# Kernel tuning notes

Measured on AMD Instinct MI355X. Metric: run time of the kernel, lower is better.

## Reference

```python
import jax, jax.numpy as jnp
import numpy as np

S, T, C, L_GNN, L_TF, H = 8, 16, 128, 3, 2, 4
B = 512
FF = 4 * C
EPS = 1e-5


def setup_inputs() -> dict:
    key = jax.random.key(0)
    ks = jax.random.split(key, 24)
    w = lambda k, shape: jax.random.normal(k, shape, jnp.float32) * 0.05
    inp = {}
    inp["xx"] = jax.random.randint(ks[0], (B, T, S, S, S), 0, 3, dtype=jnp.int32)
    inp["ss"] = jax.random.uniform(ks[1], (B, 1), jnp.float32)
    # DynamicGNNv2 params
    inp["Win"] = w(ks[2], (C, 5)); inp["b_in"] = w(ks[3], (C,))
    inp["Wl"] = w(ks[4], (L_GNN, C, C)); inp["bl"] = w(ks[5], (L_GNN, C))   # SAGEConv lin_l (neighbors)
    inp["Wr"] = w(ks[6], (L_GNN, C, C))                                      # SAGEConv lin_r (root, no bias)
    inp["ln_g"] = jnp.ones((C,), jnp.float32); inp["ln_b"] = jnp.zeros((C,), jnp.float32)  # shared LayerNorm
    # TransformerEncoder params (norm_first, relu, dropout=0 at eval)
    inp["Wqkv"] = w(ks[7], (L_TF, 3 * C, C)); inp["bqkv"] = w(ks[8], (L_TF, 3 * C))
    inp["Wo"] = w(ks[9], (L_TF, C, C)); inp["bo"] = w(ks[10], (L_TF, C))
    inp["ln1_g"] = jnp.ones((L_TF, C), jnp.float32); inp["ln1_b"] = jnp.zeros((L_TF, C), jnp.float32)
    inp["ln2_g"] = jnp.ones((L_TF, C), jnp.float32); inp["ln2_b"] = jnp.zeros((L_TF, C), jnp.float32)
    inp["W1"] = w(ks[11], (L_TF, FF, C)); inp["b1"] = w(ks[12], (L_TF, FF))
    inp["W2"] = w(ks[13], (L_TF, C, FF)); inp["b2"] = w(ks[14], (L_TF, C))
    inp["Wact"] = w(ks[15], (C, S ** 3)); inp["bact"] = w(ks[16], (C,))
    inp["Wsc"] = w(ks[17], (C, 1)); inp["bsc"] = w(ks[18], (C,))
    return inp


def layernorm(x, g, b):
    mu = x.mean(-1, keepdims=True)
    var = ((x - mu) ** 2).mean(-1, keepdims=True)
    return (x - mu) * jax.lax.rsqrt(var + EPS) * g + b


def reference(xx, ss, Win, b_in, Wl, bl, Wr, ln_g, ln_b, Wqkv, bqkv, Wo, bo,
              ln1_g, ln1_b, ln2_g, ln2_b, W1, b1, W2, b2, Wact, bact, Wsc, bsc):
    Bc = xx.shape[0]
    S3 = S ** 3
    frame0 = xx[:, 0].reshape(Bc, S3).astype(jnp.float32)            # (B,S^3)
    m = (frame0 != 0).astype(jnp.float32)                            # active-node mask
    grid = jnp.arange(S3)
    i, j, k = grid // (S * S), (grid // S) % S, grid % S
    coord = jnp.stack([i, j, k], -1).astype(jnp.float32) / (S - 1)   # (S^3,3)
    feat = jnp.concatenate([
        jnp.broadcast_to(coord, (Bc, S3, 3)),
        (frame0 / 2.0)[..., None],
        jnp.broadcast_to((ss / S)[:, None, :], (Bc, S3, 1)),
    ], -1)                                                            # (B,S^3,5)
    x = feat @ Win.T + b_in                                           # lin_in
    mm = m[..., None]
    n = m.sum(-1, keepdims=True)[..., None]                           # nodes per graph (B,1,1)
    for l in range(L_GNN):
        # complete graph (no self loops): mean over neighbors = (sum_active - self)/(N-1)
        s = (x * mm).sum(1, keepdims=True)                            # (B,1,C)
        neigh = jnp.where(n > 1, (s - x) / jnp.maximum(n - 1.0, 1.0), 0.0)
        h = neigh @ Wl[l].T + bl[l] + x @ Wr[l].T                     # SAGEConv
        x = layernorm(jax.nn.relu(h), ln_g, ln_b)
    full = x * mm                                                     # scatter-fill into dense (B,S^3,C)
    # pooling matmul: mean over each i/j/k slice -> (B,3S,C)
    poolW = jnp.concatenate([
        (i[None, :] == jnp.arange(S)[:, None]).astype(jnp.float32),
        (j[None, :] == jnp.arange(S)[:, None]).astype(jnp.float32),
        (k[None, :] == jnp.arange(S)[:, None]).astype(jnp.float32),
    ], 0)                                                             # (3S,S^3)
    gnn_emb = jnp.einsum('ps,bsc->bpc', poolW, full) / poolW.sum(1)[None, :, None]
    # transformer over past actions
    a = xx[:, 1:].reshape(Bc, T - 1, S3).astype(jnp.float32) @ Wact.T + bact
    Hd = C // H
    scale = 1.0 / np.sqrt(Hd).astype(np.float32)
    split_heads = lambda t: t.reshape(Bc, -1, H, Hd).transpose(0, 2, 1, 3)
    for l in range(L_TF):
        h1 = layernorm(a, ln1_g[l], ln1_b[l])
        q, kk, v = jnp.split(h1 @ Wqkv[l].T + bqkv[l], 3, axis=-1)
        q, kk, v = split_heads(q), split_heads(kk), split_heads(v)
        att = jax.nn.softmax(jnp.einsum('bhqd,bhkd->bhqk', q, kk) * scale, -1)
        o = jnp.einsum('bhqk,bhkd->bhqd', att, v).transpose(0, 2, 1, 3).reshape(Bc, -1, C)
        a = a + (o @ Wo[l].T + bo[l])
        h2 = layernorm(a, ln2_g[l], ln2_b[l])
        a = a + (jax.nn.relu(h2 @ W1[l].T + b1[l]) @ W2[l].T + b2[l])
    act_emb = a.mean(1)                                               # (B,C)
    mv_emb = jax.nn.relu(ss @ Wsc.T + bsc)                            # (B,C)
    return jnp.concatenate([gnn_emb, act_emb[:, None], mv_emb[:, None]], 1)  # (B,3S+2,C)
```

## Files before the change

kernel.cpp:

```cpp
#include <hip/hip_runtime.h>
#include <hip/hip_bf16.h>
#include <string.h>

typedef __hip_bfloat16 bf16;
typedef __attribute__((ext_vector_type(8))) short short8;
typedef __attribute__((ext_vector_type(4))) float f32x4;

#define Bsz 512
#define S3  512
#define Tsz 16
#define Cc  128
#define TT  15
#define EPSv 1e-5f

__device__ __forceinline__ float u2f(unsigned short u) {
    return __uint_as_float(((unsigned)u) << 16);
}
__device__ __forceinline__ float ulo(unsigned u) { return __uint_as_float(u << 16); }
__device__ __forceinline__ float uhi(unsigned u) { return __uint_as_float(u & 0xffff0000u); }
__device__ __forceinline__ unsigned short f2bu(float v) {
    bf16 h = __float2bfloat16(v);
    unsigned short u; memcpy(&u, &h, 2); return u;
}
__device__ __forceinline__ unsigned short bfr16(float a) {
    unsigned u = __float_as_uint(a);
    u = u + 0x7fffu + ((u >> 16) & 1u);
    return (unsigned short)(u >> 16);
}
__device__ __forceinline__ unsigned fpack2(float a, float b) {
    unsigned ua = __float_as_uint(a), ub = __float_as_uint(b);
    ua = ua + 0x7fffu + ((ua >> 16) & 1u);
    ub = ub + 0x7fffu + ((ub >> 16) & 1u);
    return (ua >> 16) | (ub & 0xffff0000u);
}
__device__ __forceinline__ float dot4(float4 a, float4 b) {
    return a.x*b.x + a.y*b.y + a.z*b.z + a.w*b.w;
}

__global__ __launch_bounds__(256) void k_tpack(const float* __restrict__ src,
                                               float* __restrict__ dst,
                                               int NR, int NK)
{
    __shared__ float tile[32][33];
    int k0 = blockIdx.x * 32, r0 = blockIdx.y * 32;
    int lr = threadIdx.x >> 5, lk = threadIdx.x & 31;
    for (int i = lr; i < 32; i += 8)
        tile[i][lk] = src[(size_t)(r0 + i) * NK + k0 + lk];
    __syncthreads();
    int c = threadIdx.x & 31, k4 = threadIdx.x >> 5;
    float4 v;
    v.x = tile[c][k4 * 4 + 0]; v.y = tile[c][k4 * 4 + 1];
    v.z = tile[c][k4 * 4 + 2]; v.w = tile[c][k4 * 4 + 3];
    ((float4*)dst)[(size_t)(k0 / 4 + k4) * NR + r0 + c] = v;
}

__global__ __launch_bounds__(256) void k_cvt5(
    const float* __restrict__ s0, const float* __restrict__ s1,
    const float* __restrict__ s2, const float* __restrict__ s3,
    const float* __restrict__ s4, ushort* __restrict__ dst)
{
    int i = blockIdx.x * 256 + threadIdx.x;
    if (i >= 114688) return;
    const float* src; int rel;
    if (i < 16384)      { src = s0; rel = i; }
    else if (i < 40960) { src = s1; rel = i - 16384; }
    else if (i < 49152) { src = s2; rel = i - 40960; }
    else if (i < 81920) { src = s3; rel = i - 49152; }
    else                { src = s4; rel = i - 81920; }
    float4 v = ((const float4*)src)[rel];
    ushort4 o;
    o.x = f2bu(v.x); o.y = f2bu(v.y); o.z = f2bu(v.z); o.w = f2bu(v.w);
    ((ushort4*)dst)[i] = o;
}

__global__ __launch_bounds__(256) void k_dwall(
    const int* __restrict__ xx, const float* __restrict__ Wl,
    const float* __restrict__ Wr, ushort* __restrict__ dbuf)
{
    __shared__ float pc[4];
    __shared__ float winv;
    int b = blockIdx.x, l = blockIdx.y, tid = threadIdx.x;
    const int* x0 = xx + (size_t)b * Tsz * S3;
    int c = (x0[tid] != 0) + (x0[tid + 256] != 0);
    for (int off = 32; off; off >>= 1) c += __shfl_xor(c, off, 64);
    if ((tid & 63) == 0) pc[tid >> 6] = (float)c;
    __syncthreads();
    if (tid == 0) {
        float n = pc[0] + pc[1] + pc[2] + pc[3];
        winv = (n > 1.f) ? 1.f / (n - 1.f) : 0.f;
    }
    __syncthreads();
    float inv = winv;
    const float* wl = Wl + l * 16384;
    const float* wr = Wr + l * 16384;
    ushort* dst = dbuf + (size_t)(b * 3 + l) * 32 * 512;
    for (int item = tid; item < 2048; item += 256) {
        int f = item >> 6, lane = item & 63;
        int t = f >> 2, ks = f & 3, ml = lane & 15, q = lane >> 4;
        int n = t * 16 + ml, kb = ks * 32 + q * 8;
        const float4* wlr = (const float4*)(wl + n * 128 + kb);
        const float4* wrr = (const float4*)(wr + n * 128 + kb);
        float4 a0 = wlr[0], a1 = wlr[1];
        float4 r0 = wrr[0], r1 = wrr[1];
        ushort4 o0, o1;
        o0.x = f2bu(r0.x - inv * a0.x); o0.y = f2bu(r0.y - inv * a0.y);
        o0.z = f2bu(r0.z - inv * a0.z); o0.w = f2bu(r0.w - inv * a0.w);
        o1.x = f2bu(r1.x - inv * a1.x); o1.y = f2bu(r1.y - inv * a1.y);
        o1.z = f2bu(r1.z - inv * a1.z); o1.w = f2bu(r1.w - inv * a1.w);
        ushort* dp = dst + (size_t)f * 512 + lane * 8;
        *(ushort4*)dp = o0;
        *(ushort4*)(dp + 4) = o1;
    }
}

__global__ __launch_bounds__(1024) void k_torso(
    const int* __restrict__ xx, const float* __restrict__ ss,
    const float* __restrict__ Win, const float* __restrict__ b_in,
    const ushort* __restrict__ dbuf,
    const float4* __restrict__ WlP, const float* __restrict__ blv,
    const float* __restrict__ lng, const float* __restrict__ lnb,
    float* __restrict__ out)
{
    __shared__ ushort X[512 * 136];
    __shared__ float  mC[512];
    __shared__ float  sred[16 * 128];
    __shared__ float  ssc[128];
    __shared__ float  sbase[128];
    __shared__ float  gln[128], bln[128];
    __shared__ float  scnt[16];
    __shared__ float  invS;

    int b = blockIdx.x, tid = threadIdx.x;
    int wv = tid >> 6, lane = tid & 63;
    int ml = lane & 15, quad = lane >> 4;

    {
        int g = wv, cp = lane;
        int co0 = 2 * cp, co1 = 2 * cp + 1;
        const int* x0 = xx + (size_t)b * Tsz * S3;
        float f4c = ss[b] * (1.0f / 8.0f);
        float a0 = Win[co0*5+0], a1 = Win[co0*5+1], a2 = Win[co0*5+2], a3 = Win[co0*5+3];
        float c0 = Win[co1*5+0], c1 = Win[co1*5+1], c2 = Win[co1*5+2], c3 = Win[co1*5+3];
        float ba = b_in[co0] + f4c * Win[co0*5+4];
        float bc = b_in[co1] + f4c * Win[co1*5+4];
        float sp0 = 0.f, sp1 = 0.f; int cnt = 0;
        for (int node = g; node < S3; node += 16) {
            int f0 = x0[node];
            float m = (f0 != 0) ? 1.f : 0.f;
            float ci = (float)(node >> 6) * (1.f / 7.f);
            float cj = (float)((node >> 3) & 7) * (1.f / 7.f);
            float ck = (float)(node & 7) * (1.f / 7.f);
            float ft = (float)f0 * 0.5f;
            float v0 = ba + ci * a0 + cj * a1 + ck * a2 + ft * a3;
            float v1 = bc + ci * c0 + cj * c1 + ck * c2 + ft * c3;
            ((unsigned*)(X + node * 136))[cp] = fpack2(v0, v1);
            sp0 += v0 * m; sp1 += v1 * m;
            cnt += (f0 != 0);
            if (cp == 0) mC[node] = m;
        }
        sred[g * 128 + co0] = sp0;
        sred[g * 128 + co1] = sp1;
        if (cp == 0) scnt[g] = (float)cnt;
    }
    if (tid < 128) { gln[tid] = lng[tid]; bln[tid] = lnb[tid]; }
    __syncthreads();
    if (tid == 0) {
        float n = 0.f;
#pragma unroll
        for (int g = 0; g < 16; g++) n += scnt[g];
        invS = (n > 1.f) ? 1.f / (n - 1.f) : 0.f;
    }
    __syncthreads();
    if (tid < 128) {
        float s = 0.f;
#pragma unroll
        for (int g = 0; g < 16; g++) s += sred[g * 128 + tid];
        ssc[tid] = s * invS;
    }
    __syncthreads();
    if (tid < 128) {
        float a = blv[tid];
        for (int k4 = 0; k4 < 32; k4++)
            a += dot4(*(const float4*)(ssc + k4 * 4), WlP[k4 * 384 + tid]);
        sbase[tid] = a;
    }
    __syncthreads();

    for (int l = 0; l < 3; l++) {
        f32x4 acc[8][2];
#pragma unroll
        for (int t = 0; t < 8; t++)
#pragma unroll
            for (int m = 0; m < 2; m++) acc[t][m] = (f32x4){0.f, 0.f, 0.f, 0.f};

        const ushort* dL  = dbuf + (size_t)(b * 3 + l) * 32 * 512 + lane * 8;
        const ushort* xr0 = X + (wv * 32 + ml) * 136 + quad * 8;
        const ushort* xr1 = xr0 + 16 * 136;

#pragma unroll
        for (int ks = 0; ks < 4; ks++) {
            short8 a0 = *(const short8*)(xr0 + ks * 32);
            short8 a1 = *(const short8*)(xr1 + ks * 32);
            short8 bg0[4], bg1[4];
#pragma unroll
            for (int t = 0; t < 4; t++)
                bg0[t] = *(const short8*)(dL + (size_t)(t * 4 + ks) * 512);
#pragma unroll
            for (int t = 0; t < 4; t++)
                bg1[t] = *(const short8*)(dL + (size_t)((t + 4) * 4 + ks) * 512);
#pragma unroll
            for (int t = 0; t < 4; t++) {
                acc[t][0] = __builtin_amdgcn_mfma_f32_16x16x32_bf16(a0, bg0[t], acc[t][0], 0, 0, 0);
                acc[t][1] = __builtin_amdgcn_mfma_f32_16x16x32_bf16(a1, bg0[t], acc[t][1], 0, 0, 0);
            }
#pragma unroll
            for (int t = 0; t < 4; t++) {
                acc[t + 4][0] = __builtin_amdgcn_mfma_f32_16x16x32_bf16(a0, bg1[t], acc[t + 4][0], 0, 0, 0);
                acc[t + 4][1] = __builtin_amdgcn_mfma_f32_16x16x32_bf16(a1, bg1[t], acc[t + 4][1], 0, 0, 0);
            }
        }

        float bse[8], gg[8], be[8];
#pragma unroll
        for (int t = 0; t < 8; t++) {
            bse[t] = sbase[t * 16 + ml];
            gg[t]  = gln[t * 16 + ml];
            be[t]  = bln[t * 16 + ml];
        }
        float sp[8];
#pragma unroll
        for (int t = 0; t < 8; t++) sp[t] = 0.f;
        bool last = (l == 2);

#pragma unroll
        for (int m = 0; m < 2; m++) {
#pragma unroll
            for (int r = 0; r < 4; r++) {
                int row = wv * 32 + m * 16 + quad * 4 + r;
                float s = 0.f, q = 0.f;
#pragma unroll
                for (int t = 0; t < 8; t++) {
                    float v = fmaxf(acc[t][m][r] + bse[t], 0.f);
                    acc[t][m][r] = v;
                    s += v; q += v * v;
                }
#pragma unroll
                for (int off = 1; off <= 8; off <<= 1) {
                    s += __shfl_xor(s, off, 64);
                    q += __shfl_xor(q, off, 64);
                }
                float mu = s * (1.f / 128.f);
                float rs = rsqrtf(q * (1.f / 128.f) - mu * mu + EPSv);
                float mrow = mC[row];
#pragma unroll
                for (int t = 0; t < 8; t++) {
                    float y = (acc[t][m][r] - mu) * rs * gg[t] + be[t];
                    if (last) y *= mrow;
                    else sp[t] += y * mrow;
                    X[row * 136 + t * 16 + ml] = bfr16(y);
                }
            }
        }

        if (!last) {
#pragma unroll
            for (int t = 0; t < 8; t++) {
                sp[t] += __shfl_xor(sp[t], 16, 64);
                sp[t] += __shfl_xor(sp[t], 32, 64);
            }
            if (quad == 0) {
#pragma unroll
                for (int t = 0; t < 8; t++) sred[wv * 128 + t * 16 + ml] = sp[t];
            }
            __syncthreads();
            if (tid < 128) {
                float s = 0.f;
#pragma unroll
                for (int g = 0; g < 16; g++) s += sred[g * 128 + tid];
                ssc[tid] = s * invS;
            }
            __syncthreads();
            if (tid < 128) {
                float a = blv[(l + 1) * 128 + tid];
                for (int k4 = 0; k4 < 32; k4++)
                    a += dot4(*(const float4*)(ssc + k4 * 4), WlP[k4 * 384 + (l + 1) * 128 + tid]);
                sbase[tid] = a;
            }
            __syncthreads();
        }
    }
    __syncthreads();

    if (tid < 768) {
        int c4 = tid & 31, p = tid >> 5;
        int axis = p >> 3, idx = p & 7;
        float4 sum = {0.f, 0.f, 0.f, 0.f};
        for (int t = 0; t < 64; t++) {
            int node;
            if (axis == 0)      node = idx * 64 + t;
            else if (axis == 1) node = (t >> 3) * 64 + idx * 8 + (t & 7);
            else                node = t * 8 + idx;
            uint2 pk = *(const uint2*)(X + node * 136 + c4 * 4);
            sum.x += ulo(pk.x);
            sum.y += uhi(pk.x);
            sum.z += ulo(pk.y);
            sum.w += uhi(pk.y);
        }
        float4 o;
        o.x = sum.x * (1.f / 64.f); o.y = sum.y * (1.f / 64.f);
        o.z = sum.z * (1.f / 64.f); o.w = sum.w * (1.f / 64.f);
        *(float4*)(out + (size_t)b * 26 * Cc + p * Cc + c4 * 4) = o;
    }
}

__global__ __launch_bounds__(256) void k_tf3(
    const int* __restrict__ xx, const float* __restrict__ ss,
    const ushort* __restrict__ WactB, const float* __restrict__ bact,
    const ushort* __restrict__ WqkvB, const float* __restrict__ bqkv,
    const ushort* __restrict__ WoB, const float* __restrict__ bo,
    const float* __restrict__ ln1g, const float* __restrict__ ln1b,
    const float* __restrict__ ln2g, const float* __restrict__ ln2b,
    const ushort* __restrict__ W1B, const float* __restrict__ b1v,
    const ushort* __restrict__ W2B, const float* __restrict__ b2v,
    const float* __restrict__ Wsc, const float* __restrict__ bsc,
    float* __restrict__ out)
{
    __shared__ float  As[TT * 132];
    __shared__ ushort Qs[16 * 392];
    __shared__ ushort Ab[16 * 136];
    __shared__ ushort Hs[16 * 136];
    __shared__ ushort Fs[16 * 520];
    __shared__ float  Att[60 * 16];
    __shared__ float  mu_s[TT], rs_s[TT];

    int b = blockIdx.x, tid = threadIdx.x;
    int wv = tid >> 6, lane = tid & 63;
    int ml = lane & 15, quad = lane >> 4;

    const int* xa = xx + (size_t)b * Tsz * S3 + S3;
    for (int f = tid; f < TT * 512; f += 256) {
        int t = f >> 9, s = f & 511;
        Fs[t * 520 + s] = bfr16((float)xa[t * 512 + s]);
    }
    __syncthreads();

    {
        f32x4 acc[2];
#pragma unroll
        for (int i = 0; i < 2; i++) acc[i] = (f32x4){0.f, 0.f, 0.f, 0.f};
        const ushort* ar = Fs + ml * 520 + quad * 8;
        for (int ks = 0; ks < 16; ks++) {
            short8 a = *(const short8*)(ar + ks * 32);
#pragma unroll
            for (int i = 0; i < 2; i++) {
                int n0 = (wv * 2 + i) * 16;
                short8 bfr = *(const short8*)(WactB + (size_t)(n0 + ml) * 512 + quad * 8 + ks * 32);
                acc[i] = __builtin_amdgcn_mfma_f32_16x16x32_bf16(a, bfr, acc[i], 0, 0, 0);
            }
        }
#pragma unroll
        for (int i = 0; i < 2; i++) {
            int col = (wv * 2 + i) * 16 + ml;
            float bb = bact[col];
#pragma unroll
            for (int r = 0; r < 4; r++) {
                int row = quad * 4 + r;
                if (row < TT) As[row * 132 + col] = acc[i][r] + bb;
            }
        }
    }
    __syncthreads();

    for (int l = 0; l < 2; l++) {
        const float* bq  = bqkv + l * 384;
        const float* bol = bo + l * 128;
        const float* g1  = ln1g + l * 128; const float* be1 = ln1b + l * 128;
        const float* g2  = ln2g + l * 128; const float* be2 = ln2b + l * 128;
        const float* b1l = b1v + l * 512;  const float* b2l = b2v + l * 128;

        for (int r = wv; r < TT; r += 4) {
            float2 v = *(const float2*)(As + r * 132 + lane * 2);
            float s = v.x + v.y, q = v.x * v.x + v.y * v.y;
            for (int off = 32; off; off >>= 1) {
                s += __shfl_xor(s, off, 64);
                q += __shfl_xor(q, off, 64);
            }
            if (lane == 0) {
                float mu = s * (1.f / 128.f);
                mu_s[r] = mu;
                rs_s[r] = rsqrtf(q * (1.f / 128.f) - mu * mu + EPSv);
            }
        }
        __syncthreads();
        for (int f = tid; f < TT * 64; f += 256) {
            int t = f >> 6, cp = f & 63;
            float mu = mu_s[t], rs = rs_s[t];
            float x0 = (As[t * 132 + 2 * cp]     - mu) * rs * g1[2 * cp]     + be1[2 * cp];
            float x1 = (As[t * 132 + 2 * cp + 1] - mu) * rs * g1[2 * cp + 1] + be1[2 * cp + 1];
            ((unsigned*)(Ab + t * 136))[cp] = fpack2(x0, x1);
        }
        __syncthreads();

        {
            short8 a[4];
            const ushort* ar = Ab + ml * 136 + quad * 8;
#pragma unroll
            for (int ks = 0; ks < 4; ks++) a[ks] = *(const short8*)(ar + ks * 32);
#pragma unroll
            for (int i = 0; i < 6; i++) {
                int n0 = (wv * 6 + i) * 16;
                f32x4 acc = (f32x4){0.f, 0.f, 0.f, 0.f};
                const ushort* wb = WqkvB + (size_t)(l * 384 + n0 + ml) * 128 + quad * 8;
#pragma unroll
                for (int ks = 0; ks < 4; ks++) {
                    short8 bfr = *(const short8*)(wb + ks * 32);
                    acc = __builtin_amdgcn_mfma_f32_16x16x32_bf16(a[ks], bfr, acc, 0, 0, 0);
                }
                int col = n0 + ml;
                float bb = bq[col];
#pragma unroll
                for (int r = 0; r < 4; r++) {
                    int row = quad * 4 + r;
                    if (row < TT) Qs[row * 392 + col] = bfr16(acc[r] + bb);
                }
            }
        }
        __syncthreads();

        if (tid < 60) {
            int h = tid / 15, tq = tid % 15;
            const ushort* qp = Qs + tq * 392 + h * 32;
            float sc[TT];
            float mx = -1e30f;
#pragma unroll
            for (int tk = 0; tk < TT; tk++) {
                const ushort* kp = Qs + tk * 392 + 128 + h * 32;
                float d = 0.f;
#pragma unroll
                for (int u = 0; u < 32; u += 4) {
                    uint2 qa = *(const uint2*)(qp + u);
                    uint2 ka = *(const uint2*)(kp + u);
                    d += ulo(qa.x) * ulo(ka.x) + uhi(qa.x) * uhi(ka.x)
                       + ulo(qa.y) * ulo(ka.y) + uhi(qa.y) * uhi(ka.y);
                }
                d *= 0.17677669529663689f;
                sc[tk] = d; mx = fmaxf(mx, d);
            }
            float sum = 0.f;
#pragma unroll
            for (int tk = 0; tk < TT; tk++) { float e = __expf(sc[tk] - mx); sc[tk] = e; sum += e; }
            float r = 1.f / sum;
#pragma unroll
            for (int tk = 0; tk < TT; tk++) Att[tid * 16 + tk] = sc[tk] * r;
        }
        __syncthreads();

        for (int f = tid; f < TT * 64; f += 256) {
            int t = f >> 6, cp = f & 63;
            int h = cp >> 4;
            const float* ap = Att + (h * 15 + t) * 16;
            const ushort* vp = Qs + 256 + 2 * cp;
            float a0 = 0.f, a1 = 0.f;
#pragma unroll
            for (int tk = 0; tk < TT; tk++) {
                float w = ap[tk];
                unsigned pk = *(const unsigned*)(vp + tk * 392);
                a0 += w * ulo(pk);
                a1 += w * uhi(pk);
            }
            ((unsigned*)(Hs + t * 136))[cp] = fpack2(a0, a1);
        }
        __syncthreads();

        {
            short8 a[4];
            const ushort* ar = Hs + ml * 136 + quad * 8;
#pragma unroll
            for (int ks = 0; ks < 4; ks++) a[ks] = *(const short8*)(ar + ks * 32);
#pragma unroll
            for (int i = 0; i < 2; i++) {
                int n0 = (wv * 2 + i) * 16;
                f32x4 acc = (f32x4){0.f, 0.f, 0.f, 0.f};
                const ushort* wb = WoB + (size_t)(l * 128 + n0 + ml) * 128 + quad * 8;
#pragma unroll
                for (int ks = 0; ks < 4; ks++) {
                    short8 bfr = *(const short8*)(wb + ks * 32);
                    acc = __builtin_amdgcn_mfma_f32_16x16x32_bf16(a[ks], bfr, acc, 0, 0, 0);
                }
                int col = n0 + ml;
                float bb = bol[col];
#pragma unroll
                for (int r = 0; r < 4; r++) {
                    int row = quad * 4 + r;
                    if (row < TT) As[row * 132 + col] += acc[r] + bb;
                }
            }
        }
        __syncthreads();

        for (int r = wv; r < TT; r += 4) {
            float2 v = *(const float2*)(As + r * 132 + lane * 2);
            float s = v.x + v.y, q = v.x * v.x + v.y * v.y;
            for (int off = 32; off; off >>= 1) {
                s += __shfl_xor(s, off, 64);
                q += __shfl_xor(q, off, 64);
            }
            if (lane == 0) {
                float mu = s * (1.f / 128.f);
                mu_s[r] = mu;
                rs_s[r] = rsqrtf(q * (1.f / 128.f) - mu * mu + EPSv);
            }
        }
        __syncthreads();
        for (int f = tid; f < TT * 64; f += 256) {
            int t = f >> 6, cp = f & 63;
            float mu = mu_s[t], rs = rs_s[t];
            float x0 = (As[t * 132 + 2 * cp]     - mu) * rs * g2[2 * cp]     + be2[2 * cp];
            float x1 = (As[t * 132 + 2 * cp + 1] - mu) * rs * g2[2 * cp + 1] + be2[2 * cp + 1];
            ((unsigned*)(Ab + t * 136))[cp] = fpack2(x0, x1);
        }
        __syncthreads();

        {
            short8 a[4];
            const ushort* ar = Ab + ml * 136 + quad * 8;
#pragma unroll
            for (int ks = 0; ks < 4; ks++) a[ks] = *(const short8*)(ar + ks * 32);
#pragma unroll
            for (int i = 0; i < 8; i++) {
                int n0 = (wv * 8 + i) * 16;
                f32x4 acc = (f32x4){0.f, 0.f, 0.f, 0.f};
                const ushort* wb = W1B + (size_t)(l * 512 + n0 + ml) * 128 + quad * 8;
#pragma unroll
                for (int ks = 0; ks < 4; ks++) {
                    short8 bfr = *(const short8*)(wb + ks * 32);
                    acc = __builtin_amdgcn_mfma_f32_16x16x32_bf16(a[ks], bfr, acc, 0, 0, 0);
                }
                int col = n0 + ml;
                float bb = b1l[col];
#pragma unroll
                for (int r = 0; r < 4; r++) {
                    int row = quad * 4 + r;
                    if (row < TT) Fs[row * 520 + col] = bfr16(fmaxf(acc[r] + bb, 0.f));
                }
            }
        }
        __syncthreads();

        {
            f32x4 acc[2];
#pragma unroll
            for (int i = 0; i < 2; i++) acc[i] = (f32x4){0.f, 0.f, 0.f, 0.f};
            const ushort* ar = Fs + ml * 520 + quad * 8;
            for (int ks = 0; ks < 16; ks++) {
                short8 a = *(const short8*)(ar + ks * 32);
#pragma unroll
                for (int i = 0; i < 2; i++) {
                    int n0 = (wv * 2 + i) * 16;
                    short8 bfr = *(const short8*)(W2B + (size_t)(l * 128 + n0 + ml) * 512 + quad * 8 + ks * 32);
                    acc[i] = __builtin_amdgcn_mfma_f32_16x16x32_bf16(a, bfr, acc[i], 0, 0, 0);
                }
            }
#pragma unroll
            for (int i = 0; i < 2; i++) {
                int col = (wv * 2 + i) * 16 + ml;
                float bb = b2l[col];
#pragma unroll
                for (int r = 0; r < 4; r++) {
                    int row = quad * 4 + r;
                    if (row < TT) As[row * 132 + col] += acc[i][r] + bb;
                }
            }
        }
        __syncthreads();
    }

    if (tid < 128) {
        float s = 0.f;
#pragma unroll
        for (int t = 0; t < TT; t++) s += As[t * 132 + tid];
        out[(size_t)b * 26 * Cc + 24 * Cc + tid] = s * (1.f / 15.f);
    } else if (tid < 256) {
        int co = tid - 128;
        float v = ss[b] * Wsc[co] + bsc[co];
        out[(size_t)b * 26 * Cc + 25 * Cc + co] = fmaxf(v, 0.f);
    }
}

extern "C" void kernel_launch(void* const* d_in, const int* in_sizes, int n_in,
                              void* d_out, int out_size, void* d_ws, size_t ws_size,
                              hipStream_t stream)
{
    (void)in_sizes; (void)n_in; (void)out_size; (void)ws_size;
    const int*   xx   = (const int*)d_in[0];
    const float* ss   = (const float*)d_in[1];
    const float* Win  = (const float*)d_in[2];
    const float* b_in = (const float*)d_in[3];
    const float* Wl   = (const float*)d_in[4];
    const float* bl   = (const float*)d_in[5];
    const float* Wr   = (const float*)d_in[6];
    const float* lng  = (const float*)d_in[7];
    const float* lnb  = (const float*)d_in[8];
    const float* Wqkv = (const float*)d_in[9];
    const float* bqkv = (const float*)d_in[10];
    const float* Wo   = (const float*)d_in[11];
    const float* bo   = (const float*)d_in[12];
    const float* ln1g = (const float*)d_in[13];
    const float* ln1b = (const float*)d_in[14];
    const float* ln2g = (const float*)d_in[15];
    const float* ln2b = (const float*)d_in[16];
    const float* W1   = (const float*)d_in[17];
    const float* b1   = (const float*)d_in[18];
    const float* W2   = (const float*)d_in[19];
    const float* b2   = (const float*)d_in[20];
    const float* Wact = (const float*)d_in[21];
    const float* bact = (const float*)d_in[22];
    const float* Wsc  = (const float*)d_in[23];
    const float* bsc  = (const float*)d_in[24];
    float* out = (float*)d_out;

    char* ws = (char*)d_ws;
    size_t off = 0;
    float* WlT  = (float*)(ws + off); off += 384 * 128 * 4;
    ushort* dbuf  = (ushort*)(ws + off); off += (size_t)Bsz * 3 * 32 * 512 * 2;
    ushort* WactB = (ushort*)(ws + off); off += 128 * 512 * 2;
    ushort* WqkvB = (ushort*)(ws + off); off += 768 * 128 * 2;
    ushort* WoB   = (ushort*)(ws + off); off += 256 * 128 * 2;
    ushort* W1B   = (ushort*)(ws + off); off += 1024 * 128 * 2;
    ushort* W2B   = (ushort*)(ws + off); off += 256 * 512 * 2;

    k_tpack<<<dim3(4, 12), 256, 0, stream>>>(Wl, WlT, 384, 128);
    k_cvt5<<<448, 256, 0, stream>>>(Wact, Wqkv, Wo, W1, W2, WactB);
    k_dwall<<<dim3(Bsz, 3), 256, 0, stream>>>(xx, Wl, Wr, dbuf);

    k_torso<<<Bsz, 1024, 0, stream>>>(xx, ss, Win, b_in, dbuf,
                                      (const float4*)WlT, bl, lng, lnb, out);

    k_tf3<<<Bsz, 256, 0, stream>>>(xx, ss,
                                   WactB, bact, WqkvB, bqkv, WoB, bo,
                                   ln1g, ln1b, ln2g, ln2b,
                                   W1B, b1, W2B, b2,
                                   Wsc, bsc, out);
}
```

Measured before the change: 321.5 us.

## Replace per-batch combined weight buffer with shared packed weights and two-pass MFMA

Before, a kernel built a per-batch bf16 matrix (Wr - inv*Wl) for every batch and layer, writing and then rereading about 50 MB of workspace. Now Wl and Wr are packed once into bf16, and the torso kernel runs a second set of MFMAs with the A operand scaled by -invS, so the combination happens inside the GEMM accumulation. This removes the per-batch preprocessing kernel and its memory traffic. In exchange the torso does twice the MFMA work and the extra scaling, and rounding the scaled activations to bf16 slightly changes numerics.

```diff
diff --git a/kernel.cpp b/kernel.cpp
--- a/kernel.cpp
+++ b/kernel.cpp
@@ -35,6 +35,16 @@
 }
 __device__ __forceinline__ float dot4(float4 a, float4 b) {
     return a.x*b.x + a.y*b.y + a.z*b.z + a.w*b.w;
+}
+__device__ __forceinline__ short8 scale8(short8 v, float s) {
+    const unsigned* u = (const unsigned*)&v;
+    short8 r;
+    unsigned* o = (unsigned*)&r;
+#pragma unroll
+    for (int i = 0; i < 4; i++) {
+        o[i] = fpack2(ulo(u[i]) * s, uhi(u[i]) * s);
+    }
+    return r;
 }
 
 __global__ __launch_bounds__(256) void k_tpack(const float* __restrict__ src,
@@ -73,40 +83,22 @@
     ((ushort4*)dst)[i] = o;
 }
 
-__global__ __launch_bounds__(256) void k_dwall(
-    const int* __restrict__ xx, const float* __restrict__ Wl,
-    const float* __restrict__ Wr, ushort* __restrict__ dbuf)
+__global__ __launch_bounds__(256) void k_wpack(
+    const float* __restrict__ Wl, const float* __restrict__ Wr,
+    ushort* __restrict__ WB)
 {
-    __shared__ float pc[4];
-    __shared__ float winv;
-    int b = blockIdx.x, l = blockIdx.y, tid = threadIdx.x;
-    const int* x0 = xx + (size_t)b * Tsz * S3;
-    int c = (x0[tid] != 0) + (x0[tid + 256] != 0);
-    for (int off = 32; off; off >>= 1) c += __shfl_xor(c, off, 64);
-    if ((tid & 63) == 0) pc[tid >> 6] = (float)c;
-    __syncthreads();
-    if (tid == 0) {
-        float n = pc[0] + pc[1] + pc[2] + pc[3];
-        winv = (n > 1.f) ? 1.f / (n - 1.f) : 0.f;
-    }
-    __syncthreads();
-    float inv = winv;
-    const float* wl = Wl + l * 16384;
-    const float* wr = Wr + l * 16384;
-    ushort* dst = dbuf + (size_t)(b * 3 + l) * 32 * 512;
-    for (int item = tid; item < 2048; item += 256) {
+    int l = blockIdx.x, w = blockIdx.y;
+    const float* src = (w == 0 ? Wl : Wr) + l * 16384;
+    ushort* dst = WB + (size_t)(l * 2 + w) * 32 * 512;
+    for (int item = threadIdx.x; item < 2048; item += 256) {
         int f = item >> 6, lane = item & 63;
         int t = f >> 2, ks = f & 3, ml = lane & 15, q = lane >> 4;
         int n = t * 16 + ml, kb = ks * 32 + q * 8;
-        const float4* wlr = (const float4*)(wl + n * 128 + kb);
-        const float4* wrr = (const float4*)(wr + n * 128 + kb);
-        float4 a0 = wlr[0], a1 = wlr[1];
-        float4 r0 = wrr[0], r1 = wrr[1];
+        const float4* sp = (const float4*)(src + n * 128 + kb);
+        float4 v0 = sp[0], v1 = sp[1];
         ushort4 o0, o1;
-        o0.x = f2bu(r0.x - inv * a0.x); o0.y = f2bu(r0.y - inv * a0.y);
-        o0.z = f2bu(r0.z - inv * a0.z); o0.w = f2bu(r0.w - inv * a0.w);
-        o1.x = f2bu(r1.x - inv * a1.x); o1.y = f2bu(r1.y - inv * a1.y);
-        o1.z = f2bu(r1.z - inv * a1.z); o1.w = f2bu(r1.w - inv * a1.w);
+        o0.x = f2bu(v0.x); o0.y = f2bu(v0.y); o0.z = f2bu(v0.z); o0.w = f2bu(v0.w);
+        o1.x = f2bu(v1.x); o1.y = f2bu(v1.y); o1.z = f2bu(v1.z); o1.w = f2bu(v1.w);
         ushort* dp = dst + (size_t)f * 512 + lane * 8;
         *(ushort4*)dp = o0;
         *(ushort4*)(dp + 4) = o1;
@@ -116,7 +108,7 @@
 __global__ __launch_bounds__(1024) void k_torso(
     const int* __restrict__ xx, const float* __restrict__ ss,
     const float* __restrict__ Win, const float* __restrict__ b_in,
-    const ushort* __restrict__ dbuf,
+    const ushort* __restrict__ WB,
     const float4* __restrict__ WlP, const float* __restrict__ blv,
     const float* __restrict__ lng, const float* __restrict__ lnb,
     float* __restrict__ out)
@@ -186,6 +178,8 @@
     }
     __syncthreads();
 
+    float ninv = -invS;
+
     for (int l = 0; l < 3; l++) {
         f32x4 acc[8][2];
 #pragma unroll
@@ -193,7 +187,8 @@
 #pragma unroll
             for (int m = 0; m < 2; m++) acc[t][m] = (f32x4){0.f, 0.f, 0.f, 0.f};
 
-        const ushort* dL  = dbuf + (size_t)(b * 3 + l) * 32 * 512 + lane * 8;
+        const ushort* wLp = WB + ((size_t)(l * 2 + 0) * 32) * 512 + lane * 8;
+        const ushort* wRp = WB + ((size_t)(l * 2 + 1) * 32) * 512 + lane * 8;
         const ushort* xr0 = X + (wv * 32 + ml) * 136 + quad * 8;
         const ushort* xr1 = xr0 + 16 * 136;
 
@@ -204,10 +199,28 @@
             short8 bg0[4], bg1[4];
 #pragma unroll
             for (int t = 0; t < 4; t++)
-                bg0[t] = *(const short8*)(dL + (size_t)(t * 4 + ks) * 512);
+                bg0[t] = *(const short8*)(wRp + (size_t)(t * 4 + ks) * 512);
 #pragma unroll
             for (int t = 0; t < 4; t++)
-                bg1[t] = *(const short8*)(dL + (size_t)((t + 4) * 4 + ks) * 512);
+                bg1[t] = *(const short8*)(wRp + (size_t)((t + 4) * 4 + ks) * 512);
+#pragma unroll
+            for (int t = 0; t < 4; t++) {
+                acc[t][0] = __builtin_amdgcn_mfma_f32_16x16x32_bf16(a0, bg0[t], acc[t][0], 0, 0, 0);
+                acc[t][1] = __builtin_amdgcn_mfma_f32_16x16x32_bf16(a1, bg0[t], acc[t][1], 0, 0, 0);
+            }
+#pragma unroll
+            for (int t = 0; t < 4; t++) {
+                acc[t + 4][0] = __builtin_amdgcn_mfma_f32_16x16x32_bf16(a0, bg1[t], acc[t + 4][0], 0, 0, 0);
+                acc[t + 4][1] = __builtin_amdgcn_mfma_f32_16x16x32_bf16(a1, bg1[t], acc[t + 4][1], 0, 0, 0);
+            }
+#pragma unroll
+            for (int t = 0; t < 4; t++)
+                bg0[t] = *(const short8*)(wLp + (size_t)(t * 4 + ks) * 512);
+#pragma unroll
+            for (int t = 0; t < 4; t++)
+                bg1[t] = *(const short8*)(wLp + (size_t)((t + 4) * 4 + ks) * 512);
+            a0 = scale8(a0, ninv);
+            a1 = scale8(a1, ninv);
 #pragma unroll
             for (int t = 0; t < 4; t++) {
                 acc[t][0] = __builtin_amdgcn_mfma_f32_16x16x32_bf16(a0, bg0[t], acc[t][0], 0, 0, 0);
@@ -622,7 +635,7 @@
     char* ws = (char*)d_ws;
     size_t off = 0;
     float* WlT  = (float*)(ws + off); off += 384 * 128 * 4;
-    ushort* dbuf  = (ushort*)(ws + off); off += (size_t)Bsz * 3 * 32 * 512 * 2;
+    ushort* WB    = (ushort*)(ws + off); off += (size_t)3 * 2 * 128 * 128 * 2;
     ushort* WactB = (ushort*)(ws + off); off += 128 * 512 * 2;
     ushort* WqkvB = (ushort*)(ws + off); off += 768 * 128 * 2;
     ushort* WoB   = (ushort*)(ws + off); off += 256 * 128 * 2;
@@ -631,9 +644,9 @@
 
     k_tpack<<<dim3(4, 12), 256, 0, stream>>>(Wl, WlT, 384, 128);
     k_cvt5<<<448, 256, 0, stream>>>(Wact, Wqkv, Wo, W1, W2, WactB);
-    k_dwall<<<dim3(Bsz, 3), 256, 0, stream>>>(xx, Wl, Wr, dbuf);
-
-    k_torso<<<Bsz, 1024, 0, stream>>>(xx, ss, Win, b_in, dbuf,
+    k_wpack<<<dim3(3, 2), 256, 0, stream>>>(Wl, Wr, WB);
+
+    k_torso<<<Bsz, 1024, 0, stream>>>(xx, ss, Win, b_in, WB,
                                       (const float4*)WlT, bl, lng, lnb, out);
 
     k_tf3<<<Bsz, 256, 0, stream>>>(xx, ss,
```

After: 401.0 us. 24.7% more time.
